# Kernel optimization log

Measured on AMD Instinct MI355X. Metric: run time of the kernel, lower is better.

The kernel has to match this reference:

```python
import jax, jax.numpy as jnp
import numpy as np

HIDDEN = 768
MLP_HIDDEN = 3072
HEADS = 12
HEAD_DIM = HIDDEN // HEADS

def setup_inputs() -> dict:
    key = jax.random.key(0)
    ks = jax.random.split(key, 12)
    s = 0.02
    return {
        "x": jax.random.normal(ks[0], (16, 1024, HIDDEN), dtype=jnp.float32),
        "ln1_g": jnp.ones((HIDDEN,), jnp.float32),
        "ln1_b": jnp.zeros((HIDDEN,), jnp.float32),
        "wq": jax.random.normal(ks[1], (HIDDEN, HIDDEN), jnp.float32) * s,
        "wk": jax.random.normal(ks[2], (HIDDEN, HIDDEN), jnp.float32) * s,
        "wv": jax.random.normal(ks[3], (HIDDEN, HIDDEN), jnp.float32) * s,
        "wo": jax.random.normal(ks[4], (HIDDEN, HIDDEN), jnp.float32) * s,
        "bo": jnp.zeros((HIDDEN,), jnp.float32),
        "ln2_g": jnp.ones((HIDDEN,), jnp.float32),
        "ln2_b": jnp.zeros((HIDDEN,), jnp.float32),
        "w1": jax.random.normal(ks[5], (HIDDEN, MLP_HIDDEN), jnp.float32) * s,
        "b1": jnp.zeros((MLP_HIDDEN,), jnp.float32),
        "w2": jax.random.normal(ks[6], (MLP_HIDDEN, HIDDEN), jnp.float32) * s,
        "b2": jnp.zeros((HIDDEN,), jnp.float32),
    }

def _layernorm(x, g, b, eps=1e-5):
    mu = jnp.mean(x, axis=-1, keepdims=True)
    var = jnp.mean(jnp.square(x - mu), axis=-1, keepdims=True)
    return (x - mu) * jax.lax.rsqrt(var + eps) * g + b

def reference(x, ln1_g, ln1_b, wq, wk, wv, wo, bo, ln2_g, ln2_b, w1, b1, w2, b2):
    b, n, _ = x.shape
    h, d = HEADS, HEAD_DIM
    scale = d ** -0.5
    # Attention branch
    xn = _layernorm(x, ln1_g, ln1_b)
    q = (xn @ wq.T).reshape(b, n, h, d).transpose(0, 2, 1, 3)  # bhnd
    k = (xn @ wk.T).reshape(b, n, h, d).transpose(0, 2, 1, 3)
    v = (xn @ wv.T).reshape(b, n, h, d).transpose(0, 2, 1, 3)
    score = jax.nn.softmax(jnp.einsum('bhif,bhjf->bhij', q, k) * scale, axis=-1)
    attn = jnp.einsum('bhij,bhjf->bihf', score, v).reshape(b, n, h * d)
    x = attn @ wo.T + bo + x
    # MLP branch
    xn = _layernorm(x, ln2_g, ln2_b)
    hdn = jax.nn.gelu(xn @ w1 + b1, approximate=False)
    x = hdn @ w2 + b2 + x
    return x
```

## Files before the change

kernel.cpp:

```cpp
#include <hip/hip_runtime.h>
#include <hip/hip_bf16.h>

#define HIDDEN 768
#define MLPH   3072
#define HEADS  12
#define HD     64
#define SEQ    1024
#define BATCH  16
#define MTOT   (BATCH*SEQ)

typedef __attribute__((ext_vector_type(8))) short  short8;
typedef __attribute__((ext_vector_type(4))) short  short4x;
typedef __attribute__((ext_vector_type(8))) __bf16 bf16x8;
typedef __attribute__((ext_vector_type(4))) float  floatx4;

#define CL2 0.18033688011112042f

__device__ inline short f2bf(float f) {
  __hip_bfloat16 h = __float2bfloat16(f);
  return *reinterpret_cast<short*>(&h);
}

__device__ inline floatx4 mfma_bf16(short8 a, short8 b, floatx4 c) {
  return __builtin_amdgcn_mfma_f32_16x16x32_bf16(
      __builtin_bit_cast(bf16x8, a), __builtin_bit_cast(bf16x8, b), c, 0, 0, 0);
}

__device__ inline void gl_lds16(const short* g, short* l) {
  __builtin_amdgcn_global_load_lds(
      (const __attribute__((address_space(1))) unsigned int*)g,
      (__attribute__((address_space(3))) unsigned int*)l, 16, 0, 0);
}

__global__ __launch_bounds__(256) void conv_weights(
    const float* __restrict__ wq, const float* __restrict__ wk,
    const float* __restrict__ wv, const float* __restrict__ wo,
    const float* __restrict__ w1, const float* __restrict__ w2,
    short* __restrict__ wqkvb, short* __restrict__ wob,
    short* __restrict__ w1t,   short* __restrict__ w2t)
{
  int i = blockIdx.x * 256 + threadIdx.x;
  const int HH = HIDDEN * HIDDEN;
  if (i < HH) {
    wqkvb[i]        = f2bf(wq[i]);
    wqkvb[HH + i]   = f2bf(wk[i]);
    wqkvb[2*HH + i] = f2bf(wv[i]);
    wob[i]          = f2bf(wo[i]);
  }
  if (i < HIDDEN * MLPH) {
    int n = i / HIDDEN, k = i % HIDDEN;
    w1t[i] = f2bf(w1[(size_t)k * MLPH + n]);
    int n2 = i / MLPH, k2 = i % MLPH;
    w2t[i] = f2bf(w2[(size_t)k2 * HIDDEN + n2]);
  }
}

__global__ __launch_bounds__(256) void ln_kernel(
    const float* __restrict__ x, const float* __restrict__ g,
    const float* __restrict__ b, short* __restrict__ out)
{
  int row = blockIdx.x;
  const float* xr = x + (size_t)row * HIDDEN;
  int t = threadIdx.x;
  float v0 = xr[t], v1 = xr[t + 256], v2 = xr[t + 512];
  float s  = v0 + v1 + v2;
  float s2 = v0*v0 + v1*v1 + v2*v2;
  for (int off = 32; off > 0; off >>= 1) {
    s  += __shfl_down(s, off);
    s2 += __shfl_down(s2, off);
  }
  __shared__ float red[8];
  __shared__ float stats[2];
  int wave = t >> 6;
  if ((t & 63) == 0) { red[wave] = s; red[4 + wave] = s2; }
  __syncthreads();
  if (t == 0) {
    float S  = red[0] + red[1] + red[2] + red[3];
    float S2 = red[4] + red[5] + red[6] + red[7];
    float mu  = S * (1.0f / HIDDEN);
    float var = S2 * (1.0f / HIDDEN) - mu * mu;
    stats[0] = mu;
    stats[1] = rsqrtf(var + 1e-5f);
  }
  __syncthreads();
  float mu = stats[0], rs = stats[1];
  short* orow = out + (size_t)row * HIDDEN;
  orow[t]       = f2bf((v0 - mu) * rs * g[t]       + b[t]);
  orow[t + 256] = f2bf((v1 - mu) * rs * g[t + 256] + b[t + 256]);
  orow[t + 512] = f2bf((v2 - mu) * rs * g[t + 512] + b[t + 512]);
}

template<int OUTMODE , bool BIAS, bool GELU_E, bool RES,
         bool SCALEQ = false>
__global__ __launch_bounds__(512, 2) void gemm_bt2(
    const short* __restrict__ A, const short* __restrict__ B,
    const float* __restrict__ bias, const float* __restrict__ res,
    void* __restrict__ out, int M, int N, int K)
{
  __shared__ alignas(16) short As[2][8192];
  __shared__ alignas(16) short Bs[2][8192];

  int tid = threadIdx.x;
  int lane = tid & 63, wave = tid >> 6;
  int wr = wave >> 2, wc = wave & 3;
  int quad = lane >> 4, lc = lane & 15;

  int nbx = gridDim.x;
  int nwg = nbx * gridDim.y;
  int orig = blockIdx.y * nbx + blockIdx.x;
  int q8 = nwg >> 3, r8 = nwg & 7;
  int xcd = orig & 7, sub = orig >> 3;
  int wg = (xcd < r8 ? xcd * (q8 + 1) : r8 * (q8 + 1) + (xcd - r8) * q8) + sub;
  int m0 = (wg / nbx) * 256;
  int n0 = (wg % nbx) * 256;

  int srow = tid >> 2;
  int skb  = (tid & 3) ^ ((srow >> 1) & 3);
  const short* ga0 = A + (size_t)(m0 + srow) * K + skb * 8;
  const short* ga1 = ga0 + (size_t)128 * K;
  const short* gb0 = B + (size_t)(n0 + srow) * K + skb * 8;
  const short* gb1 = gb0 + (size_t)128 * K;
  int lbase = wave * 512;

#define STAGE(KO, BUF) {                              \
    gl_lds16(ga0 + (KO), &As[BUF][lbase]);            \
    gl_lds16(ga1 + (KO), &As[BUF][4096 + lbase]);     \
    gl_lds16(gb0 + (KO), &Bs[BUF][lbase]);            \
    gl_lds16(gb1 + (KO), &Bs[BUF][4096 + lbase]);     \
  }

  floatx4 acc[8][4];
#pragma unroll
  for (int i = 0; i < 8; ++i)
#pragma unroll
    for (int j = 0; j < 4; ++j) acc[i][j] = floatx4{0.f, 0.f, 0.f, 0.f};

  int apos = (quad ^ ((lc >> 1) & 3)) * 8;
  int arow = wr * 128 + lc;
  int brow = wc * 64 + lc;

#define COMPUTE(BUF) {                                                  \
    const short* as_ = As[BUF];                                         \
    const short* bs_ = Bs[BUF];                                         \
    short8 af[8], bfr[4];                                               \
    _Pragma("unroll")                                                   \
    for (int i = 0; i < 8; ++i)                                         \
      af[i] = *(const short8*)&as_[(arow + i * 16) * 32 + apos];        \
    _Pragma("unroll")                                                   \
    for (int j = 0; j < 4; ++j)                                         \
      bfr[j] = *(const short8*)&bs_[(brow + j * 16) * 32 + apos];       \
    _Pragma("unroll")                                                   \
    for (int i = 0; i < 8; ++i)                                         \
      _Pragma("unroll")                                                 \
      for (int j = 0; j < 4; ++j)                                       \
        acc[i][j] = mfma_bf16(af[i], bfr[j], acc[i][j]);                \
  }

  int NT = K >> 5;

  STAGE(0, 0);
  __syncthreads();

  for (int t = 0; t < NT; t += 2) {
    STAGE((t + 1) * 32, 1);
    COMPUTE(0);
    __syncthreads();
    if (t + 2 < NT) STAGE((t + 2) * 32, 0);
    COMPUTE(1);
    __syncthreads();
  }
#undef STAGE
#undef COMPUTE

#pragma unroll
  for (int i = 0; i < 8; ++i)
#pragma unroll
    for (int j = 0; j < 4; ++j)
#pragma unroll
      for (int r = 0; r < 4; ++r) {
        int row = m0 + wr * 128 + i * 16 + quad * 4 + r;
        int col = n0 + wc * 64 + j * 16 + lc;
        float v = acc[i][j][r];
        if (BIAS)   v += bias[col];
        if (GELU_E) v = 0.5f * v * (1.0f + erff(v * 0.70710678118f));
        if (RES)    v += res[(size_t)row * N + col];
        if (SCALEQ && col < HIDDEN) v *= CL2;
        if (OUTMODE == 1) ((short*)out)[(size_t)row * N + col] = f2bf(v);
        else              ((float*)out)[(size_t)row * N + col] = v;
      }
}

__global__ __launch_bounds__(256) void vtrans_kernel(
    const short* __restrict__ qkv, short* __restrict__ vtg)
{
  int kt = blockIdx.x, h = blockIdx.y, b = blockIdx.z;
  int t = threadIdx.x;
  __shared__ short Vl[64][72];
  const short* vb = qkv + (size_t)(b * SEQ + kt * 64) * 2304 + 1536 + h * 64;
  int row = t >> 2, seg = t & 3;
  short8 r0 = *(const short8*)(vb + (size_t)row * 2304 + seg * 16);
  short8 r1 = *(const short8*)(vb + (size_t)row * 2304 + seg * 16 + 8);
  *(short8*)&Vl[row][seg * 16]     = r0;
  *(short8*)&Vl[row][seg * 16 + 8] = r1;
  __syncthreads();
  int ks = t >> 7, d = (t & 127) >> 1, hb = t & 1;
  short8 w0;
#pragma unroll
  for (int u = 0; u < 8; ++u) {
    int blk = hb * 2 + (u >> 3), j = u & 7;
    int ksrc = ks * 32 + (blk ^ ((d >> 1) & 3)) * 8 + j;
    w0[u] = Vl[ksrc][d];
  }
  short8 w1;
#pragma unroll
  for (int u = 8; u < 16; ++u) {
    int blk = hb * 2 + (u >> 3), j = u & 7;
    int ksrc = ks * 32 + (blk ^ ((d >> 1) & 3)) * 8 + j;
    w1[u - 8] = Vl[ksrc][d];
  }
  short* o = vtg + ((size_t)((b * HEADS + h) * 16 + kt)) * 4096 + t * 16;
  *(short8*)o       = w0;
  *(short8*)(o + 8) = w1;
}

__global__ __launch_bounds__(512) void attn_kernel(
    const short* __restrict__ qkv, const short* __restrict__ vtg,
    short* __restrict__ out)
{
  int qt = blockIdx.x;
  int h  = blockIdx.y;
  int b  = blockIdx.z;
  int tid = threadIdx.x, lane = tid & 63, wave = tid >> 6;
  int quad = lane >> 4, lc = lane & 15;

  __shared__ alignas(16) short Qs[2 * 128 * 32];
  __shared__ alignas(16) short Ks[2 * 64 * 32];
  __shared__ alignas(16) short Vs[2 * 64 * 32];
  __shared__ alignas(16) short Ps[8][16 * 72];

  const int LDQ = 3 * HIDDEN;
  const short* qb = qkv + (size_t)(b * SEQ) * LDQ + h * HD;
  const short* kb = qb + HIDDEN;
  const short* vt = vtg + (size_t)((b * HEADS + h) * 16) * 4096;

  {
    int row = tid >> 2, blk = tid & 3;
    int kblk = blk ^ ((row >> 1) & 3);
#pragma unroll
    for (int t = 0; t < 2; ++t) {
      const short* g = qb + (size_t)(qt * 128 + row) * LDQ + t * 32 + kblk * 8;
      gl_lds16(g, &Qs[t * 4096 + wave * 512]);
    }
  }
  __syncthreads();

  int pos = quad ^ ((lc >> 1) & 3);
  short8 aq[2];
#pragma unroll
  for (int ks = 0; ks < 2; ++ks)
    aq[ks] = *(const short8*)&Qs[ks * 4096 + (wave * 16 + lc) * 32 + pos * 8];

  floatx4 oacc[4];
#pragma unroll
  for (int n2 = 0; n2 < 4; ++n2) oacc[n2] = floatx4{0.f, 0.f, 0.f, 0.f};
  float lsum = 0.f;

  int srow = (tid >> 2) & 63;
  int sks  = tid >> 8;
  int skb  = (tid & 3) ^ ((srow >> 1) & 3);
  const short* kg0 = kb + (size_t)srow * LDQ + sks * 32 + skb * 8;
  const short* vg0 = vt + tid * 8;
  short* pw = &Ps[wave][0];

  for (int kt = 0; kt < 16; ++kt) {
    gl_lds16(kg0 + (size_t)(kt * 64) * LDQ, &Ks[wave * 512]);
    gl_lds16(vg0 + kt * 4096, &Vs[wave * 512]);
    __syncthreads();

    floatx4 sacc[4];
#pragma unroll
    for (int m2 = 0; m2 < 4; ++m2) sacc[m2] = floatx4{0.f, 0.f, 0.f, 0.f};
#pragma unroll
    for (int ks = 0; ks < 2; ++ks) {
#pragma unroll
      for (int m2 = 0; m2 < 4; ++m2) {
        short8 ak = *(const short8*)&Ks[ks * 2048 + (m2 * 16 + lc) * 32 + pos * 8];
        sacc[m2] = mfma_bf16(ak, aq[ks], sacc[m2]);
      }
    }

#pragma unroll
    for (int m2 = 0; m2 < 4; ++m2) {
      float p0 = exp2f(sacc[m2][0]);
      float p1 = exp2f(sacc[m2][1]);
      float p2 = exp2f(sacc[m2][2]);
      float p3 = exp2f(sacc[m2][3]);
      lsum += (p0 + p1) + (p2 + p3);
      short4x pk;
      pk[0] = f2bf(p0); pk[1] = f2bf(p1); pk[2] = f2bf(p2); pk[3] = f2bf(p3);
      *(short4x*)&pw[lc * 72 + m2 * 16 + quad * 4] = pk;
    }
    asm volatile("s_waitcnt lgkmcnt(0)" ::: "memory");
    __builtin_amdgcn_sched_barrier(0);

#pragma unroll
    for (int ks = 0; ks < 2; ++ks) {
      short8 ap = *(const short8*)&pw[lc * 72 + (ks * 4 + quad) * 8];
#pragma unroll
      for (int n2 = 0; n2 < 4; ++n2) {
        short8 bv = *(const short8*)&Vs[ks * 2048 + (n2 * 16 + lc) * 32 + pos * 8];
        oacc[n2] = mfma_bf16(ap, bv, oacc[n2]);
      }
    }
    __syncthreads();
  }

  float rs = lsum;
  rs += __shfl_xor(rs, 16);
  rs += __shfl_xor(rs, 32);
#pragma unroll
  for (int r = 0; r < 4; ++r) {
    float inv = 1.0f / __shfl(rs, quad * 4 + r);
    int row = b * SEQ + qt * 128 + wave * 16 + quad * 4 + r;
#pragma unroll
    for (int n2 = 0; n2 < 4; ++n2) {
      int col = h * HD + n2 * 16 + lc;
      out[(size_t)row * HIDDEN + col] = f2bf(oacc[n2][r] * inv);
    }
  }
}

extern "C" void kernel_launch(void* const* d_in, const int* in_sizes, int n_in,
                              void* d_out, int out_size, void* d_ws, size_t ws_size,
                              hipStream_t stream) {
  const float* x    = (const float*)d_in[0];
  const float* ln1g = (const float*)d_in[1];
  const float* ln1b = (const float*)d_in[2];
  const float* wq   = (const float*)d_in[3];
  const float* wk   = (const float*)d_in[4];
  const float* wv   = (const float*)d_in[5];
  const float* wo   = (const float*)d_in[6];
  const float* bo   = (const float*)d_in[7];
  const float* ln2g = (const float*)d_in[8];
  const float* ln2b = (const float*)d_in[9];
  const float* w1   = (const float*)d_in[10];
  const float* b1   = (const float*)d_in[11];
  const float* w2   = (const float*)d_in[12];
  const float* b2   = (const float*)d_in[13];

  auto rup = [](size_t b) { return (b + 255) & ~(size_t)255; };
  const size_t wbytes = rup((size_t)3 * HIDDEN * HIDDEN * 2) +
                        rup((size_t)HIDDEN * HIDDEN * 2) +
                        rup((size_t)MLPH * HIDDEN * 2) +
                        rup((size_t)HIDDEN * MLPH * 2);

  int R = SEQ;
  const int cands[4] = {16384, 8192, 4096, 2048};
  for (int i = 0; i < 4; ++i) {
    size_t need = wbytes + rup((size_t)cands[i] * 1536) + rup((size_t)cands[i] * 6144)
                         + rup((size_t)cands[i] * 1536);
    if (need <= ws_size) { R = cands[i]; break; }
  }

  char* ws = (char*)d_ws;
  size_t off = 0;
  auto alloc = [&](size_t bytes) {
    char* p = ws + off;
    off += (bytes + 255) & ~(size_t)255;
    return p;
  };
  short* wqkvb = (short*)alloc((size_t)3 * HIDDEN * HIDDEN * 2);
  short* wob   = (short*)alloc((size_t)HIDDEN * HIDDEN * 2);
  short* w1t   = (short*)alloc((size_t)MLPH * HIDDEN * 2);
  short* w2t   = (short*)alloc((size_t)HIDDEN * MLPH * 2);
  short* slotA = (short*)alloc((size_t)R * 1536);
  short* bigR  = (short*)alloc((size_t)R * 6144);
  short* vtg   = (short*)alloc((size_t)R * 1536);

  conv_weights<<<(HIDDEN * MLPH + 255) / 256, 256, 0, stream>>>(
      wq, wk, wv, wo, w1, w2, wqkvb, wob, w1t, w2t);

  const int nch = MTOT / R;
  for (int c = 0; c < nch; ++c) {
    const float* xc  = x + (size_t)c * R * HIDDEN;
    float*       x2c = (float*)d_out + (size_t)c * R * HIDDEN;

    ln_kernel<<<R, 256, 0, stream>>>(xc, ln1g, ln1b, slotA);
    gemm_bt2<1, false, false, false, true>
        <<<dim3((3 * HIDDEN) / 256, R / 256), 512, 0, stream>>>(
        slotA, wqkvb, nullptr, nullptr, bigR, R, 3 * HIDDEN, HIDDEN);
    vtrans_kernel<<<dim3(16, HEADS, R / SEQ), 256, 0, stream>>>(bigR, vtg);
    attn_kernel<<<dim3(SEQ / 128, HEADS, R / SEQ), 512, 0, stream>>>(
        bigR, vtg, slotA);
    gemm_bt2<0, true, false, true>
        <<<dim3(HIDDEN / 256, R / 256), 512, 0, stream>>>(
        slotA, wob, bo, xc, x2c, R, HIDDEN, HIDDEN);
    ln_kernel<<<R, 256, 0, stream>>>(x2c, ln2g, ln2b, slotA);
    gemm_bt2<1, true, true, false>
        <<<dim3(MLPH / 256, R / 256), 512, 0, stream>>>(
        slotA, w1t, b1, nullptr, bigR, R, MLPH, HIDDEN);
    gemm_bt2<0, true, false, true>
        <<<dim3(HIDDEN / 256, R / 256), 512, 0, stream>>>(
        bigR, w2t, b2, x2c, x2c, R, HIDDEN, MLPH);
  }
}
```

Measured before the change: 616.9 us.

## Deepen GEMM pipeline to four LDS stages with split A/B loads and priority

Replaces the double-buffered GEMM main loop with a four-buffer ring that keeps three K-tiles in flight. The A and B staging is split across two half-iterations, synchronized with explicit vmcnt/lgkmcnt waits and raw s_barrier, and the MFMA phases run at raised wave priority (ping-pong style). The aim is to hide global-to-LDS latency and interleave memory and matrix work across waves. LDS use doubles to 128KB per workgroup, which likely drops occupancy from 2 workgroups per CU to 1. The hand-written wait counts also risk races if the load counts are wrong.

```diff
diff --git a/kernel.cpp b/kernel.cpp
--- a/kernel.cpp
+++ b/kernel.cpp
@@ -97,8 +97,8 @@
     const float* __restrict__ bias, const float* __restrict__ res,
     void* __restrict__ out, int M, int N, int K)
 {
-  __shared__ alignas(16) short As[2][8192];
-  __shared__ alignas(16) short Bs[2][8192];
+  __shared__ alignas(16) short As[4][8192];
+  __shared__ alignas(16) short Bs[4][8192];
 
   int tid = threadIdx.x;
   int lane = tid & 63, wave = tid >> 6;
@@ -122,11 +122,15 @@
   const short* gb1 = gb0 + (size_t)128 * K;
   int lbase = wave * 512;
 
-#define STAGE(KO, BUF) {                              \
-    gl_lds16(ga0 + (KO), &As[BUF][lbase]);            \
-    gl_lds16(ga1 + (KO), &As[BUF][4096 + lbase]);     \
-    gl_lds16(gb0 + (KO), &Bs[BUF][lbase]);            \
-    gl_lds16(gb1 + (KO), &Bs[BUF][4096 + lbase]);     \
+#define STAGE_A(T) {                                        \
+    const int _b = (T) & 3;                                 \
+    gl_lds16(ga0 + (size_t)(T) * 32, &As[_b][lbase]);       \
+    gl_lds16(ga1 + (size_t)(T) * 32, &As[_b][4096 + lbase]);\
+  }
+#define STAGE_B(T) {                                        \
+    const int _b = (T) & 3;                                 \
+    gl_lds16(gb0 + (size_t)(T) * 32, &Bs[_b][lbase]);       \
+    gl_lds16(gb1 + (size_t)(T) * 32, &Bs[_b][4096 + lbase]);\
   }
 
   floatx4 acc[8][4];
@@ -139,38 +143,58 @@
   int arow = wr * 128 + lc;
   int brow = wc * 64 + lc;
 
-#define COMPUTE(BUF) {                                                  \
-    const short* as_ = As[BUF];                                         \
-    const short* bs_ = Bs[BUF];                                         \
-    short8 af[8], bfr[4];                                               \
-    _Pragma("unroll")                                                   \
-    for (int i = 0; i < 8; ++i)                                         \
-      af[i] = *(const short8*)&as_[(arow + i * 16) * 32 + apos];        \
-    _Pragma("unroll")                                                   \
-    for (int j = 0; j < 4; ++j)                                         \
-      bfr[j] = *(const short8*)&bs_[(brow + j * 16) * 32 + apos];       \
-    _Pragma("unroll")                                                   \
-    for (int i = 0; i < 8; ++i)                                         \
-      _Pragma("unroll")                                                 \
-      for (int j = 0; j < 4; ++j)                                       \
-        acc[i][j] = mfma_bf16(af[i], bfr[j], acc[i][j]);                \
-  }
-
   int NT = K >> 5;
 
-  STAGE(0, 0);
-  __syncthreads();
-
-  for (int t = 0; t < NT; t += 2) {
-    STAGE((t + 1) * 32, 1);
-    COMPUTE(0);
-    __syncthreads();
-    if (t + 2 < NT) STAGE((t + 2) * 32, 0);
-    COMPUTE(1);
-    __syncthreads();
-  }
-#undef STAGE
-#undef COMPUTE
+  STAGE_A(0); STAGE_B(0); STAGE_A(1); STAGE_B(1); STAGE_A(2); STAGE_B(2);
+  asm volatile("s_waitcnt vmcnt(8)" ::: "memory");
+  __builtin_amdgcn_s_barrier();
+  asm volatile("" ::: "memory");
+
+  for (int t = 0; t < NT; ++t) {
+    const short* as_ = As[t & 3];
+    const short* bs_ = Bs[t & 3];
+    short8 af[8], bfr[4];
+    if (t + 3 < NT) STAGE_A(t + 3);
+#pragma unroll
+    for (int i = 0; i < 4; ++i)
+      af[i] = *(const short8*)&as_[(arow + i * 16) * 32 + apos];
+#pragma unroll
+    for (int j = 0; j < 4; ++j)
+      bfr[j] = *(const short8*)&bs_[(brow + j * 16) * 32 + apos];
+    __builtin_amdgcn_s_barrier();
+    asm volatile("s_waitcnt lgkmcnt(0)" ::: "memory");
+    __builtin_amdgcn_sched_barrier(0);
+    __builtin_amdgcn_s_setprio(1);
+#pragma unroll
+    for (int i = 0; i < 4; ++i)
+#pragma unroll
+      for (int j = 0; j < 4; ++j)
+        acc[i][j] = mfma_bf16(af[i], bfr[j], acc[i][j]);
+    __builtin_amdgcn_s_setprio(0);
+    asm volatile("" ::: "memory");
+    if (t + 3 < NT) STAGE_B(t + 3);
+#pragma unroll
+    for (int i = 4; i < 8; ++i)
+      af[i] = *(const short8*)&as_[(arow + i * 16) * 32 + apos];
+    __builtin_amdgcn_s_barrier();
+    asm volatile("s_waitcnt lgkmcnt(0)" ::: "memory");
+    __builtin_amdgcn_sched_barrier(0);
+    __builtin_amdgcn_s_setprio(1);
+#pragma unroll
+    for (int i = 4; i < 8; ++i)
+#pragma unroll
+      for (int j = 0; j < 4; ++j)
+        acc[i][j] = mfma_bf16(af[i], bfr[j], acc[i][j]);
+    __builtin_amdgcn_s_setprio(0);
+    int ahead = NT - 2 - t;
+    if (ahead >= 2)      asm volatile("s_waitcnt vmcnt(8)" ::: "memory");
+    else if (ahead == 1) asm volatile("s_waitcnt vmcnt(4)" ::: "memory");
+    else if (ahead == 0) asm volatile("s_waitcnt vmcnt(0)" ::: "memory");
+    __builtin_amdgcn_s_barrier();
+    asm volatile("" ::: "memory");
+  }
+#undef STAGE_A
+#undef STAGE_B
 
 #pragma unroll
   for (int i = 0; i < 8; ++i)
```

After: 658.0 us. +6.7%, slower.
